# Kernel tuning notes

Hardware: AMD Instinct MI355X
Metric: run time of the kernel (lower is better)

Reference implementation:

```python
import jax, jax.numpy as jnp
import numpy as np
from jax import lax

N_HEADS = 12
HEAD_DIM = 64
ALPHA = 4.0  # spikingjelly surrogate.Sigmoid default alpha
EPS = 1e-5   # BatchNorm1d default eps

@jax.custom_vjp
def _heaviside(v):
    return (v >= 0.0).astype(v.dtype)

def _heaviside_fwd(v):
    return _heaviside(v), v

def _heaviside_bwd(v, g):
    sg = jax.nn.sigmoid(ALPHA * v)
    return (g * ALPHA * sg * (1.0 - sg),)

_heaviside.defvjp(_heaviside_fwd, _heaviside_bwd)

def if_node(x):
    """Multi-step IFNode (v_threshold=1, hard reset to 0), scan over leading T dim."""
    def step(v, xt):
        v = v + xt                      # integrate
        s = _heaviside(v - 1.0)         # fire
        v = (1.0 - s) * v               # hard reset: spiked neurons -> 0
        return v, s
    _, spikes = lax.scan(step, jnp.zeros_like(x[0]), x)
    return spikes

def bn1d(x):
    """Fresh (training-mode) BatchNorm1d over (T, S, D) with channels=S;
    affine weight=1, bias=0 at init, so pure normalization over axes (0,2)."""
    mean = x.mean(axis=(0, 2), keepdims=True)
    var = x.var(axis=(0, 2), keepdims=True)  # biased variance, as torch BN uses
    return (x - mean) * lax.rsqrt(var + EPS)

def setup_inputs() -> dict:
    key = jax.random.key(0)
    ks = jax.random.split(key, 5)
    T, S, D = 4, 2048, 768
    x = jax.random.normal(ks[0], (T, S, D), dtype=jnp.float32)
    scale = 0.02
    wq = jax.random.normal(ks[1], (D, D), dtype=jnp.float32) * scale
    wk = jax.random.normal(ks[2], (D, D), dtype=jnp.float32) * scale
    wv = jax.random.normal(ks[3], (D, D), dtype=jnp.float32) * scale
    wo = jax.random.normal(ks[4], (D, D), dtype=jnp.float32) * scale
    return {"x": x, "wq": wq, "wk": wk, "wv": wv, "wo": wo, "cur_pos": S}

def reference(x, wq, wk, wv, wo, cur_pos):
    T, S, D = x.shape
    tmp = if_node(x)                    # init_spike
    Q = tmp @ wq
    V = tmp @ wv
    K = tmp @ wk
    Q = if_node(bn1d(Q))                # spike_q(bnq(Q))
    V = if_node(bn1d(V))                # spike_v(bnv(V))
    K = if_node(bn1d(K))                # spike_k(bnk(K))
    # (T, S, H, hd) -> (T, H, S, hd)
    Qh = Q.reshape(T, S, N_HEADS, HEAD_DIM).transpose(0, 2, 1, 3)
    Vh = V.reshape(T, S, N_HEADS, HEAD_DIM).transpose(0, 2, 1, 3)
    Kh = K.reshape(T, S, N_HEADS, HEAD_DIM).transpose(0, 2, 1, 3)
    QK = (Qh * Kh).sum(axis=2, keepdims=True)   # (T, H, 1, hd)
    QK = if_node(QK)                    # talking_heads
    QKV = Vh * QK                       # (T, H, S, hd)
    QKV = QKV.transpose(0, 2, 1, 3).reshape(T, S, D)
    return bn1d(QKV @ wo)
```

## Files before the change

kernel.cpp:

```cpp
#include <hip/hip_runtime.h>

#define T_ 4
#define S_ 2048
#define D_ 768
#define SD_ (S_ * D_)
#define TSD_ (T_ * SD_)
#define H_ 12
#define HD_ 64
#define PLANE_BYTES 2359296u

typedef int int32x4 __attribute__((ext_vector_type(4)));

__device__ __forceinline__ void cp16(unsigned char* lds, const unsigned char* g) {
    __builtin_amdgcn_global_load_lds(
        (const __attribute__((address_space(1))) unsigned int*)g,
        (__attribute__((address_space(3))) unsigned int*)lds, 16, 0, 0);
}

__device__ __forceinline__ size_t frag_addr(int m, int d) {
    return ((size_t)(m >> 4) * 12 + (d >> 6)) * 1024 +
           (size_t)(((d >> 4) & 3) * 256 + (m & 15) * 16 + (d & 15));
}

__global__ __launch_bounds__(256) void k_prep_all(const float* __restrict__ wq,
                                                  const float* __restrict__ wk,
                                                  const float* __restrict__ wv,
                                                  const float* __restrict__ wo,
                                                  const float* __restrict__ x,
                                                  unsigned char* __restrict__ Bp,
                                                  unsigned char* __restrict__ Sx,
                                                  unsigned int* __restrict__ QKp) {
    __shared__ __align__(16) unsigned char shm[50176];
    int tid = threadIdx.x;
    if (blockIdx.y < 4) {
        unsigned char* wl = shm;
        const float* W = (blockIdx.y == 0) ? wq : (blockIdx.y == 1) ? wk
                       : (blockIdx.y == 2) ? wv : wo;
        unsigned char* out = Bp + (size_t)blockIdx.y * PLANE_BYTES;
        int c = blockIdx.x;
        int kb = c % 12;
        int nbg = c / 12;
        int k_loc = tid >> 2;
        int n_base = (tid & 3) * 4;
        float4 w4 = *(const float4*)(
            W + (size_t)(kb * 64 + k_loc) * D_ + nbg * 16 + n_base);
        float wsv[4] = {w4.x, w4.y, w4.z, w4.w};
#pragma unroll
        for (int j = 0; j < 4; j++) {
            int n_loc = n_base + j;
            int u = (int)rintf(wsv[j] * 1073741824.0f);
#pragma unroll
            for (int p = 0; p < 4; p++) {
                wl[p * 1024 + (n_loc + 16 * (k_loc >> 4)) * 16 + (k_loc & 15)] =
                    (unsigned char)(u & 255);
                u = (u + 128) >> 8;
            }
        }
        __syncthreads();
        int p = tid >> 6;
        int lane = tid & 63;
        uint4 val = *(const uint4*)&wl[p * 1024 + lane * 16];
        *(uint4*)(out + (size_t)((p * 48 + nbg) * 12 + kb) * 1024 + lane * 16) =
            val;
    } else {
        if (blockIdx.x >= 128) {
            if (blockIdx.x == 128) {
                for (int i = tid; i < 1536; i += 256) QKp[i] = 0u;
            }
            return;
        }
        int s0 = blockIdx.x * 16;
        uint4* sx = (uint4*)shm;
        for (int p = 0; p < 3; p++) {
            int pi = tid + p * 256;
            int sl = pi / 48;
            int dc = pi % 48;
            int d0 = dc * 16;
            double v[16];
#pragma unroll
            for (int j = 0; j < 16; j++) v[j] = 0.0;
#pragma unroll
            for (int t = 0; t < T_; t++) {
                union { uint4 u; unsigned char b[16]; } sp;
#pragma unroll
                for (int q = 0; q < 4; q++) {
                    float4 xt = *(const float4*)(
                        x + (size_t)t * SD_ + (size_t)(s0 + sl) * D_ + d0 +
                        q * 4);
                    float xs[4] = {xt.x, xt.y, xt.z, xt.w};
#pragma unroll
                    for (int j = 0; j < 4; j++) {
                        int jj = q * 4 + j;
                        v[jj] += (double)xs[j];
                        unsigned char ss = (v[jj] >= 1.0) ? 1 : 0;
                        sp.b[jj] = ss;
                        if (ss) v[jj] = 0.0;
                    }
                }
                sx[(t * 16 + sl) * 49 + dc] = sp.u;
            }
        }
        __syncthreads();
#pragma unroll
        for (int j = 0; j < 12; j++) {
            int f = tid + j * 256;
            int t = f / 768;
            int u = f % 768;
            int sl = u & 15;
            int dc = ((u >> 6) << 2) | ((u >> 4) & 3);
            uint4 val = sx[(t * 16 + sl) * 49 + dc];
            *(uint4*)(Sx + ((size_t)(t * 128 + (s0 >> 4)) * 12) * 1024 +
                      (size_t)u * 16) = val;
        }
    }
}

__global__ __launch_bounds__(256, 2) void k_gemm_i8(
    const unsigned char* __restrict__ A,
    const unsigned char* __restrict__ Bp,
    const unsigned int* __restrict__ Mp,
    float* __restrict__ C0, float* __restrict__ C1, float* __restrict__ C2,
    int bzoff) {
    int z = blockIdx.z;
    const unsigned char* B = Bp + (size_t)(bzoff + z) * PLANE_BYTES;
    float* C = (z == 0) ? C0 : (z == 1) ? C1 : C2;

    __shared__ __align__(16) unsigned char bsm[2 * 32768];
    __shared__ __align__(16) unsigned int maskw[192];

    int tid = threadIdx.x;
    int lane = tid & 63;
    int w = tid >> 6;
    int wm = w >> 1;
    int wn = w & 1;
    int row0 = blockIdx.x * 128;
    int tI = row0 >> 11;
    int n0 = blockIdx.y * 64;
    int nbg0 = blockIdx.y * 4;
    int col = lane & 15;
    int quad = lane >> 4;

    int32x4 zerov = {0, 0, 0, 0};
    int32x4 acc[4][2][4];
#pragma unroll
    for (int mb = 0; mb < 4; mb++)
#pragma unroll
        for (int nb = 0; nb < 2; nb++)
#pragma unroll
            for (int p = 0; p < 4; p++) acc[mb][nb][p] = zerov;

    const unsigned char* Ab =
        A + (size_t)((row0 >> 4) + wm * 4) * 12 * 1024 + lane * 16;

    auto stageB = [&](int buf, int kb2) {
        unsigned char* bb = bsm + buf * 32768;
#pragma unroll
        for (int kk = 0; kk < 2; kk++)
#pragma unroll
            for (int qi = 0; qi < 4; qi++) {
                int q = w * 4 + qi;
                int p = q >> 2, nb = q & 3;
                cp16(bb + kk * 16384 + q * 1024,
                     B + (size_t)((p * 48 + nbg0 + nb) * 12 + 2 * kb2 + kk) *
                             1024 + lane * 16);
            }
    };

    stageB(0, 0);
    if (Mp && tid < 192) {
        const unsigned long long* Qb = (const unsigned long long*)Mp;
        unsigned long long m = 0;
#pragma unroll
        for (int c = 0; c < 16; c++) m |= Qb[(c * 4 + tI) * 12 + (tid >> 4)];
        unsigned int nib =
            (unsigned int)((m >> (4 * (tid & 15))) & 0xFull);
        maskw[tid] = (nib & 1u) | ((nib & 2u) << 7) | ((nib & 4u) << 14) |
                     ((nib & 8u) << 21);
    }
    int32x4 a[2][4];
#pragma unroll
    for (int mb = 0; mb < 4; mb++)
        a[0][mb] = *(const int32x4*)(Ab + (size_t)(mb * 12) * 1024);
    __syncthreads();

    for (int kb2 = 0; kb2 < 6; kb2++) {
        int cur = kb2 & 1;
        if (kb2 < 5) stageB(1 - cur, kb2 + 1);
#pragma unroll
        for (int kbh = 0; kbh < 2; kbh++) {
            int kb = kb2 * 2 + kbh;
            if (kb < 11) {
#pragma unroll
                for (int mb = 0; mb < 4; mb++)
                    a[(kb + 1) & 1][mb] = *(const int32x4*)(
                        Ab + (size_t)(mb * 12 + kb + 1) * 1024);
            }
            int32x4 af[4];
#pragma unroll
            for (int mb = 0; mb < 4; mb++) af[mb] = a[kb & 1][mb];
            if (Mp) {
                int32x4 mv = *(const int32x4*)(
                    (const unsigned char*)maskw + kb * 64 + quad * 16);
#pragma unroll
                for (int mb = 0; mb < 4; mb++) af[mb] &= mv;
            }
            const unsigned char* bb = bsm + cur * 32768 + kbh * 16384;
#pragma unroll
            for (int p = 0; p < 4; p++)
#pragma unroll
                for (int nb = 0; nb < 2; nb++) {
                    int32x4 bf = *(const int32x4*)(
                        bb + (size_t)(p * 4 + wn * 2 + nb) * 1024 + lane * 16);
#pragma unroll
                    for (int mb = 0; mb < 4; mb++)
                        acc[mb][nb][p] = __builtin_amdgcn_mfma_i32_16x16x64_i8(
                            af[mb], bf, acc[mb][nb][p], 0, 0, 0);
                }
        }
        __syncthreads();
    }

#pragma unroll
    for (int mb = 0; mb < 4; mb++)
#pragma unroll
        for (int nb = 0; nb < 2; nb++)
#pragma unroll
            for (int r = 0; r < 4; r++) {
                double td = (double)acc[mb][nb][0][r]
                          + 256.0 * (double)acc[mb][nb][1][r]
                          + 65536.0 * (double)acc[mb][nb][2][r]
                          + 16777216.0 * (double)acc[mb][nb][3][r];
                float v = (float)(td * (1.0 / 1073741824.0));
                int rr = row0 + wm * 64 + mb * 16 + quad * 4 + r;
                int cc = n0 + wn * 32 + nb * 16 + col;
                C[(size_t)rr * D_ + cc] = v;
            }
}

__global__ __launch_bounds__(256) void k_bnif_qk(const float* __restrict__ Qf,
                                                 const float* __restrict__ Kf,
                                                 const float* __restrict__ Vf,
                                                 unsigned char* __restrict__ Vs,
                                                 unsigned int* __restrict__ QKp) {
    int s = blockIdx.x;
    __shared__ float buf[3][T_][D_];
    __shared__ double red[4][6];
    __shared__ unsigned char spkV[T_ * D_];
    __shared__ double stats[3][2];

    int tid = threadIdx.x;
    int lane = tid & 63, wv = tid >> 6;
    const float* Xs[3] = {Qf, Kf, Vf};
    double sum[3] = {0.0, 0.0, 0.0}, sumsq[3] = {0.0, 0.0, 0.0};
#pragma unroll
    for (int y = 0; y < 3; y++) {
#pragma unroll
        for (int i = 0; i < 3; i++) {
            int idx = i * 256 + tid;
            int t = idx / 192;
            int c = idx - t * 192;
            float4 v = *(const float4*)(
                Xs[y] + (size_t)t * SD_ + (size_t)s * D_ + c * 4);
            *(float4*)&buf[y][t][c * 4] = v;
            sum[y] += ((double)v.x + (double)v.y) +
                      ((double)v.z + (double)v.w);
            sumsq[y] += ((double)v.x * v.x + (double)v.y * v.y) +
                        ((double)v.z * v.z + (double)v.w * v.w);
        }
    }
#pragma unroll
    for (int off = 32; off > 0; off >>= 1) {
#pragma unroll
        for (int y = 0; y < 3; y++) {
            sum[y] += __shfl_down(sum[y], off);
            sumsq[y] += __shfl_down(sumsq[y], off);
        }
    }
    if (lane == 0) {
#pragma unroll
        for (int y = 0; y < 3; y++) {
            red[wv][y] = sum[y];
            red[wv][3 + y] = sumsq[y];
        }
    }
    __syncthreads();
    if (tid < 3) {
        double s4 = red[0][tid] + red[1][tid] + red[2][tid] + red[3][tid];
        double q4 = red[0][3 + tid] + red[1][3 + tid] + red[2][3 + tid] +
                    red[3][3 + tid];
        double mean = s4 / 3072.0;
        double var = q4 / 3072.0 - mean * mean;
        stats[tid][0] = mean;
        stats[tid][1] = 1.0 / sqrt(var + 1e-5);
    }
    __syncthreads();

    unsigned long long* QKb =
        (unsigned long long*)QKp + ((size_t)(s & 15) * 4) * 12;
#pragma unroll
    for (int i = 0; i < 3; i++) {
        int d = i * 256 + tid;
        unsigned char qs[T_], ks[T_];
#pragma unroll
        for (int y = 0; y < 3; y++) {
            double mean = stats[y][0], rstd = stats[y][1];
            double v = 0.0;
#pragma unroll
            for (int t = 0; t < T_; t++) {
                double xn = ((double)buf[y][t][d] - mean) * rstd;
                v += xn;
                unsigned char sp = (v >= 1.0) ? 1 : 0;
                if (y == 0) qs[t] = sp;
                else if (y == 1) ks[t] = sp;
                else spkV[t * D_ + d] = sp;
                if (sp) v = 0.0;
            }
        }
#pragma unroll
        for (int t = 0; t < T_; t++) {
            unsigned long long b = __ballot(qs[t] & ks[t]);
            if (lane == 0 && b) atomicOr(QKb + t * 12 + (i * 4 + wv), b);
        }
    }
    __syncthreads();

    if (tid < 192) {
        int tt = tid / 48, gg = tid % 48;
        uint4 val = *(const uint4*)&spkV[tt * D_ + gg * 16];
        size_t dst = ((size_t)(tt * 128 + (s >> 4)) * 12 + (gg >> 2)) * 1024 +
                     (size_t)((gg & 3) * 256 + (s & 15) * 16);
        *(uint4*)(Vs + dst) = val;
    }
}

__global__ __launch_bounds__(256) void k_bn_out(const float* __restrict__ Xin,
                                                float* __restrict__ out) {
    int s = blockIdx.x;
    __shared__ double red[4][2];
    __shared__ double st[2];
    int tid = threadIdx.x;
    int lane = tid & 63, wv = tid >> 6;
    float4 vv[3];
    double sum = 0.0, sumsq = 0.0;
#pragma unroll
    for (int i = 0; i < 3; i++) {
        int idx = i * 256 + tid;
        int t = idx / 192, c = idx - t * 192;
        float4 v = *(const float4*)(
            Xin + (size_t)t * SD_ + (size_t)s * D_ + c * 4);
        vv[i] = v;
        sum += ((double)v.x + (double)v.y) + ((double)v.z + (double)v.w);
        sumsq += ((double)v.x * v.x + (double)v.y * v.y) +
                 ((double)v.z * v.z + (double)v.w * v.w);
    }
#pragma unroll
    for (int off = 32; off > 0; off >>= 1) {
        sum += __shfl_down(sum, off);
        sumsq += __shfl_down(sumsq, off);
    }
    if (lane == 0) { red[wv][0] = sum; red[wv][1] = sumsq; }
    __syncthreads();
    if (tid == 0) {
        double s4 = red[0][0] + red[1][0] + red[2][0] + red[3][0];
        double q4 = red[0][1] + red[1][1] + red[2][1] + red[3][1];
        double mean = s4 / 3072.0;
        double var = q4 / 3072.0 - mean * mean;
        st[0] = mean;
        st[1] = 1.0 / sqrt(var + 1e-5);
    }
    __syncthreads();
    double mean = st[0], rstd = st[1];
#pragma unroll
    for (int i = 0; i < 3; i++) {
        int idx = i * 256 + tid;
        int t = idx / 192, c = idx - t * 192;
        float4 o;
        o.x = (float)(((double)vv[i].x - mean) * rstd);
        o.y = (float)(((double)vv[i].y - mean) * rstd);
        o.z = (float)(((double)vv[i].z - mean) * rstd);
        o.w = (float)(((double)vv[i].w - mean) * rstd);
        *(float4*)(out + (size_t)t * SD_ + (size_t)s * D_ + c * 4) = o;
    }
}

extern "C" void kernel_launch(void* const* d_in, const int* in_sizes, int n_in,
                              void* d_out, int out_size, void* d_ws,
                              size_t ws_size, hipStream_t stream) {
    const float* x  = (const float*)d_in[0];
    const float* wq = (const float*)d_in[1];
    const float* wk = (const float*)d_in[2];
    const float* wv = (const float*)d_in[3];
    const float* wo = (const float*)d_in[4];
    float* out = (float*)d_out;

    float* ws  = (float*)d_ws;
    float* Qf  = ws;
    float* Kf  = ws + (size_t)TSD_;
    float* Vf  = ws + (size_t)2 * TSD_;
    unsigned int* QKp = (unsigned int*)(ws + (size_t)3 * TSD_);
    unsigned char* Sx = (unsigned char*)(QKp + 12288);
    unsigned char* Vs = Sx + (size_t)TSD_;
    unsigned char* Bp = Vs + (size_t)TSD_;

    k_prep_all<<<dim3(576, 5), 256, 0, stream>>>(wq, wk, wv, wo, x, Bp, Sx,
                                                 QKp);
    k_gemm_i8<<<dim3(64, 12, 3), 256, 0, stream>>>(Sx, Bp, nullptr,
                                                   Qf, Kf, Vf, 0);
    k_bnif_qk<<<S_, 256, 0, stream>>>(Qf, Kf, Vf, Vs, QKp);
    k_gemm_i8<<<dim3(64, 12, 1), 256, 0, stream>>>(Vs, Bp, QKp, Qf, Qf, Qf, 3);
    k_bn_out<<<S_, 256, 0, stream>>>(Qf, out);
}
```

Before: 202.8 us.

## Stage A and B tiles through triple-buffered LDS pipeline in int8 GEMM

The int8 GEMM now stages both the A fragments and the B tiles into LDS with async global_load_lds copies. It uses three rotating buffers, staying two k-steps ahead with explicit vmcnt waits and a single barrier per k-step. Previously A was loaded directly from global memory into registers with only one-step register prefetch, and B used a double buffer. The change also raises wave priority around the MFMA section, aiming to hide global latency better. The cost is more LDS per block, which could lower occupancy, plus reliance on hand-tuned waitcnt counts for correctness.

```diff
diff --git a/kernel.cpp b/kernel.cpp
--- a/kernel.cpp
+++ b/kernel.cpp
@@ -8,6 +8,7 @@
 #define H_ 12
 #define HD_ 64
 #define PLANE_BYTES 2359296u
+#define KBUF 24576
 
 typedef int int32x4 __attribute__((ext_vector_type(4)));
 
@@ -125,7 +126,7 @@
     const unsigned char* B = Bp + (size_t)(bzoff + z) * PLANE_BYTES;
     float* C = (z == 0) ? C0 : (z == 1) ? C1 : C2;
 
-    __shared__ __align__(16) unsigned char bsm[2 * 32768];
+    __shared__ __align__(16) unsigned char lds3[3 * KBUF];
     __shared__ __align__(16) unsigned int maskw[192];
 
     int tid = threadIdx.x;
@@ -149,24 +150,25 @@
 #pragma unroll
             for (int p = 0; p < 4; p++) acc[mb][nb][p] = zerov;
 
-    const unsigned char* Ab =
-        A + (size_t)((row0 >> 4) + wm * 4) * 12 * 1024 + lane * 16;
-
-    auto stageB = [&](int buf, int kb2) {
-        unsigned char* bb = bsm + buf * 32768;
-#pragma unroll
-        for (int kk = 0; kk < 2; kk++)
-#pragma unroll
-            for (int qi = 0; qi < 4; qi++) {
-                int q = w * 4 + qi;
-                int p = q >> 2, nb = q & 3;
-                cp16(bb + kk * 16384 + q * 1024,
-                     B + (size_t)((p * 48 + nbg0 + nb) * 12 + 2 * kb2 + kk) *
-                             1024 + lane * 16);
-            }
+    const unsigned char* Ag = A + (size_t)(row0 >> 4) * 12 * 1024 + lane * 16;
+    const unsigned char* Bg = B + lane * 16;
+
+    auto stage = [&](int buf, int kb) {
+        unsigned char* dst = lds3 + buf * KBUF;
+#pragma unroll
+        for (int i = 0; i < 2; i++) {
+            int mc = w * 2 + i;
+            cp16(dst + mc * 1024, Ag + (size_t)(mc * 12 + kb) * 1024);
+        }
+#pragma unroll
+        for (int qi = 0; qi < 4; qi++) {
+            int q = w * 4 + qi;
+            int p = q >> 2, nb = q & 3;
+            cp16(dst + 8192 + q * 1024,
+                 Bg + (size_t)((p * 48 + nbg0 + nb) * 12 + kb) * 1024);
+        }
     };
 
-    stageB(0, 0);
     if (Mp && tid < 192) {
         const unsigned long long* Qb = (const unsigned long long*)Mp;
         unsigned long long m = 0;
@@ -177,47 +179,51 @@
         maskw[tid] = (nib & 1u) | ((nib & 2u) << 7) | ((nib & 4u) << 14) |
                      ((nib & 8u) << 21);
     }
-    int32x4 a[2][4];
-#pragma unroll
-    for (int mb = 0; mb < 4; mb++)
-        a[0][mb] = *(const int32x4*)(Ab + (size_t)(mb * 12) * 1024);
-    __syncthreads();
-
-    for (int kb2 = 0; kb2 < 6; kb2++) {
-        int cur = kb2 & 1;
-        if (kb2 < 5) stageB(1 - cur, kb2 + 1);
-#pragma unroll
-        for (int kbh = 0; kbh < 2; kbh++) {
-            int kb = kb2 * 2 + kbh;
-            if (kb < 11) {
+    stage(0, 0);
+    stage(1, 1);
+    asm volatile("s_waitcnt lgkmcnt(0)" ::: "memory");
+    __builtin_amdgcn_sched_barrier(0);
+    __builtin_amdgcn_s_barrier();
+    __builtin_amdgcn_sched_barrier(0);
+
+    auto kstep = [&](int k, int cur, int nxt) {
+        if (k < 11) asm volatile("s_waitcnt vmcnt(6)" ::: "memory");
+        else        asm volatile("s_waitcnt vmcnt(0)" ::: "memory");
+        __builtin_amdgcn_sched_barrier(0);
+        __builtin_amdgcn_s_barrier();
+        __builtin_amdgcn_sched_barrier(0);
+        if (k < 10) stage(nxt, k + 2);
+        const unsigned char* Ab = lds3 + cur * KBUF;
+        const unsigned char* Bb = Ab + 8192;
+        __builtin_amdgcn_s_setprio(1);
+        int32x4 af[4];
+#pragma unroll
+        for (int mb = 0; mb < 4; mb++)
+            af[mb] = *(const int32x4*)(Ab + (wm * 4 + mb) * 1024 + lane * 16);
+        if (Mp) {
+            int32x4 mv = *(const int32x4*)(
+                (const unsigned char*)maskw + k * 64 + quad * 16);
+#pragma unroll
+            for (int mb = 0; mb < 4; mb++) af[mb] &= mv;
+        }
+#pragma unroll
+        for (int p = 0; p < 4; p++)
+#pragma unroll
+            for (int nb = 0; nb < 2; nb++) {
+                int32x4 bf = *(const int32x4*)(
+                    Bb + (p * 4 + wn * 2 + nb) * 1024 + lane * 16);
 #pragma unroll
                 for (int mb = 0; mb < 4; mb++)
-                    a[(kb + 1) & 1][mb] = *(const int32x4*)(
-                        Ab + (size_t)(mb * 12 + kb + 1) * 1024);
-            }
-            int32x4 af[4];
-#pragma unroll
-            for (int mb = 0; mb < 4; mb++) af[mb] = a[kb & 1][mb];
-            if (Mp) {
-                int32x4 mv = *(const int32x4*)(
-                    (const unsigned char*)maskw + kb * 64 + quad * 16);
-#pragma unroll
-                for (int mb = 0; mb < 4; mb++) af[mb] &= mv;
-            }
-            const unsigned char* bb = bsm + cur * 32768 + kbh * 16384;
-#pragma unroll
-            for (int p = 0; p < 4; p++)
-#pragma unroll
-                for (int nb = 0; nb < 2; nb++) {
-                    int32x4 bf = *(const int32x4*)(
-                        bb + (size_t)(p * 4 + wn * 2 + nb) * 1024 + lane * 16);
-#pragma unroll
-                    for (int mb = 0; mb < 4; mb++)
-                        acc[mb][nb][p] = __builtin_amdgcn_mfma_i32_16x16x64_i8(
-                            af[mb], bf, acc[mb][nb][p], 0, 0, 0);
-                }
-        }
-        __syncthreads();
+                    acc[mb][nb][p] = __builtin_amdgcn_mfma_i32_16x16x64_i8(
+                        af[mb], bf, acc[mb][nb][p], 0, 0, 0);
+            }
+        __builtin_amdgcn_s_setprio(0);
+    };
+
+    for (int kt = 0; kt < 12; kt += 3) {
+        kstep(kt + 0, 0, 2);
+        kstep(kt + 1, 1, 0);
+        kstep(kt + 2, 2, 1);
     }
 
 #pragma unroll
```

New measurement: 209.0 us. 1.03x slower.
